# Optimization experiments

Measured on AMD Instinct MI355X. Metric: run time of the kernel, lower is better.

## Reference

```python
import jax, jax.numpy as jnp
import numpy as np

B, S, D, H = 2, 2048, 1024, 16
HD = D // H  # head_dim = 64


def setup_inputs() -> dict:
    key = jax.random.key(0)
    k1, k2, k3 = jax.random.split(key, 3)
    x = jax.random.normal(k1, (B, S, D), dtype=jnp.float32)
    W_qkv = jax.random.normal(k2, (D, 3 * D), dtype=jnp.float32) * (D ** -0.5)
    b_qkv = jnp.zeros((3 * D,), dtype=jnp.float32)
    W_proj = jax.random.normal(k3, (D, D), dtype=jnp.float32) * (D ** -0.5)
    b_proj = jnp.zeros((D,), dtype=jnp.float32)
    return {"x": x, "W_qkv": W_qkv, "b_qkv": b_qkv, "W_proj": W_proj, "b_proj": b_proj}


def reference(x, W_qkv, b_qkv, W_proj, b_proj):
    b, s, d = x.shape
    scale = HD ** -0.5
    qkv = x @ W_qkv + b_qkv                       # [B,S,3D]
    q, k, v = jnp.split(qkv, 3, axis=-1)
    # [B,S,D] -> [B,H,S,HD]
    def to_heads(t):
        return t.reshape(b, s, H, HD).transpose(0, 2, 1, 3)
    q, k, v = map(to_heads, (q, k, v))
    scores = jnp.einsum('bhqd,bhkd->bhqk', q, k) * scale  # [B,H,S,S]
    causal = jnp.triu(jnp.ones((s, s), dtype=bool), k=1)
    scores = jnp.where(causal[None, None], -jnp.inf, scores)
    attn = jax.nn.softmax(scores, axis=-1)
    out = jnp.einsum('bhqk,bhkd->bhqd', attn, v)  # [B,H,S,HD]
    out = out.transpose(0, 2, 1, 3).reshape(b, s, d)
    return out @ W_proj + b_proj
```

## Files before the change

### kernel.cpp

```cpp
#include <hip/hip_runtime.h>

using frag_t = __attribute__((ext_vector_type(8))) short;
using f32x4  = __attribute__((ext_vector_type(4))) float;

#define L2E 1.4426950408889634f

#if __has_builtin(__builtin_amdgcn_exp2f)
#define EXP2(x) __builtin_amdgcn_exp2f(x)
#else
#define EXP2(x) exp2f(x)
#endif

constexpr int B_  = 2, S_ = 2048, D_ = 1024, H_ = 16, HD_ = 64;
constexpr int M_  = B_ * S_;
constexpr float QSCALE = 0.125f * L2E;

__device__ __forceinline__ ushort f2bf(float f) {
  union { float f; unsigned u; } v; v.f = f;
  unsigned u = v.u;
  unsigned r = (u + 0x7FFFu + ((u >> 16) & 1u)) >> 16;
  return (ushort)r;
}
__device__ __forceinline__ unsigned pk_bf2(float a, float b) {
  unsigned ua = __float_as_uint(a) + 0x8000u;
  unsigned ub = __float_as_uint(b) + 0x8000u;
  return (ua >> 16) | (ub & 0xFFFF0000u);
}

__device__ __forceinline__ void gld_lds16(const ushort* g, ushort* l) {
  __builtin_amdgcn_global_load_lds((const __attribute__((address_space(1))) void*)g,
                                   (__attribute__((address_space(3))) void*)l, 16, 0, 0);
}

__global__ __launch_bounds__(256) void k_prep(
    const float* __restrict__ x, const float* __restrict__ Wqkv,
    const float* __restrict__ Wproj,
    ushort* __restrict__ Xbf, ushort* __restrict__ Wqt, ushort* __restrict__ Wpt) {
  int blk = blockIdx.x, tid = threadIdx.x;
  if (blk < 1024) {
    size_t base = (size_t)blk * 4096 + tid * 4;
    #pragma unroll
    for (int i = 0; i < 4; ++i) {
      float4 f = *(const float4*)(x + base + i * 1024);
      ushort4 o;
      o.x = f2bf(f.x); o.y = f2bf(f.y); o.z = f2bf(f.z); o.w = f2bf(f.w);
      *(ushort4*)(Xbf + base + i * 1024) = o;
    }
  } else {
    __shared__ float tile[64][65];
    const float* in; ushort* out; int N, K, bx, by;
    if (blk < 1024 + 768) { int b2 = blk - 1024; in = Wqkv;  out = Wqt; N = 3072; K = 1024; bx = b2 % 48; by = b2 / 48; }
    else                  { int b2 = blk - 1792; in = Wproj; out = Wpt; N = 1024; K = 1024; bx = b2 % 16; by = b2 / 16; }
    int n0 = bx * 64, k0 = by * 64;
    int tx = tid & 63, ty = tid >> 6;
    #pragma unroll
    for (int i = 0; i < 16; ++i)
      tile[ty + i * 4][tx] = in[(size_t)(k0 + ty + i * 4) * N + n0 + tx];
    __syncthreads();
    #pragma unroll
    for (int i = 0; i < 16; ++i)
      out[(size_t)(n0 + ty + i * 4) * K + k0 + tx] = f2bf(tile[tx][ty + i * 4]);
  }
}

template <int EPI>
__global__ __launch_bounds__(256) void k_gemm(
    const ushort* __restrict__ A, const ushort* __restrict__ Bt,
    const float* __restrict__ bias,
    ushort* __restrict__ Qo, ushort* __restrict__ Ko, ushort* __restrict__ Vo,
    float* __restrict__ Co, int N, int K) {
  constexpr int BM = (EPI == 0) ? 128 : 64;
  constexpr int BN = 64, BK = 64;
  constexpr int MI = (EPI == 0) ? 4 : 2, NI = 2;
  __shared__ ushort smem[(BM + BN) * BK];
  ushort* As = smem;
  ushort* Bs = smem + BM * BK;
  int tid  = threadIdx.x;
  int lane = tid & 63, wave = tid >> 6;
  int quad = lane >> 4, li = lane & 15;
  int mbase = (wave >> 1) * (MI * 16);
  int nbase = (wave & 1) * 32;
  int m0 = blockIdx.y * BM, n0 = blockIdx.x * BN;
  int srow = lane >> 3;
  int scol = ((lane & 7) ^ srow) * 8;
  f32x4 acc[MI][NI] = {};
  for (int k0 = 0; k0 < K; k0 += BK) {
    if (EPI == 0) {
      #pragma unroll
      for (int i = 0; i < 4; ++i) {
        int rbase = i * 32 + wave * 8;
        gld_lds16(&A[(size_t)(m0 + rbase + srow) * K + k0 + scol], &As[rbase * BK]);
      }
    } else {
      #pragma unroll
      for (int i = 0; i < 2; ++i) {
        int rbase = wave * 16 + i * 8;
        gld_lds16(&A[(size_t)(m0 + rbase + srow) * K + k0 + scol], &As[rbase * BK]);
      }
    }
    #pragma unroll
    for (int i = 0; i < 2; ++i) {
      int rbase = wave * 16 + i * 8;
      gld_lds16(&Bt[(size_t)(n0 + rbase + srow) * K + k0 + scol], &Bs[rbase * BK]);
    }
    __syncthreads();
    #pragma unroll
    for (int ks = 0; ks < 2; ++ks) {
      frag_t af[MI], bf[NI];
      #pragma unroll
      for (int mi = 0; mi < MI; ++mi)
        af[mi] = *(const frag_t*)&As[(mbase + mi * 16 + li) * BK + (((ks * 4 + quad) ^ (li & 7)) * 8)];
      #pragma unroll
      for (int ni = 0; ni < NI; ++ni)
        bf[ni] = *(const frag_t*)&Bs[(nbase + ni * 16 + li) * BK + (((ks * 4 + quad) ^ (li & 7)) * 8)];
      #pragma unroll
      for (int mi = 0; mi < MI; ++mi)
        #pragma unroll
        for (int ni = 0; ni < NI; ++ni)
          acc[mi][ni] = __builtin_amdgcn_mfma_f32_16x16x32_bf16(af[mi], bf[ni], acc[mi][ni], 0, 0, 0);
    }
    __syncthreads();
  }
  if (EPI == 1) {
    #pragma unroll
    for (int mi = 0; mi < MI; ++mi)
      #pragma unroll
      for (int ni = 0; ni < NI; ++ni) {
        int gcol = n0 + nbase + ni * 16 + li;
        float bv = bias[gcol];
        #pragma unroll
        for (int r = 0; r < 4; ++r) {
          int grow = m0 + mbase + mi * 16 + quad * 4 + r;
          Co[(size_t)grow * N + gcol] = acc[mi][ni][r] + bv;
        }
      }
  } else {
    int which = (n0 + nbase) >> 10;
    if (which < 2) {
      #pragma unroll
      for (int mi = 0; mi < MI; ++mi)
        #pragma unroll
        for (int ni = 0; ni < NI; ++ni) {
          int gcol = n0 + nbase + ni * 16 + li;
          float bv = bias[gcol];
          #pragma unroll
          for (int r = 0; r < 4; ++r) {
            int grow = m0 + mbase + mi * 16 + quad * 4 + r;
            float v = acc[mi][ni][r] + bv;
            int d = gcol & 1023, h = d >> 6, hd = d & 63;
            int b = grow >> 11, s = grow & 2047;
            size_t bh = (size_t)b * H_ + h;
            if (which == 0) Qo[(bh * S_ + s) * HD_ + hd] = f2bf(v * QSCALE);
            else            Ko[(bh * S_ + s) * HD_ + hd] = f2bf(v);
          }
        }
    } else {
      ushort* vlds = smem + wave * (32 * 72);
      #pragma unroll
      for (int ni = 0; ni < NI; ++ni) {
        float bv = bias[n0 + nbase + ni * 16 + li];
        #pragma unroll
        for (int mi = 0; mi < MI; ++mi)
          #pragma unroll
          for (int r = 0; r < 4; ++r)
            vlds[(ni * 16 + li) * 72 + 16 * quad + 4 * r + mi] = f2bf(acc[mi][ni][r] + bv);
      }
      int hgrp = (((n0 & 1023) + nbase) >> 6);
      int hd0  = (n0 + nbase) & 63;
      int b = m0 >> 11;
      int s0 = (m0 & 2047) + mbase;
      size_t vbase = (size_t)(b * H_ + hgrp) * HD_ * S_;
      #pragma unroll
      for (int i = 0; i < 4; ++i) {
        int row = i * 8 + (lane >> 3);
        int col = (lane & 7) * 8;
        *(uint4*)&Vo[vbase + (size_t)(hd0 + row) * S_ + s0 + col] = *(const uint4*)&vlds[row * 72 + col];
      }
    }
  }
}

__global__ __launch_bounds__(256) void k_attn(
    const ushort* __restrict__ Q, const ushort* __restrict__ K,
    const ushort* __restrict__ Vt, ushort* __restrict__ O) {
  __shared__ ushort Kbuf[2][64 * 64];
  __shared__ ushort Vbuf[2][64 * 64];
  __shared__ ushort Plds[4 * 16 * 64];
  int lane = threadIdx.x & 63, wave = threadIdx.x >> 6;
  int quad = lane >> 4, li = lane & 15;
  int bh = blockIdx.x;
  int qb = 31 - (int)blockIdx.y;
  int b = bh >> 4, h = bh & 15;
  int q0 = qb * 64 + wave * 16;
  const ushort* Qb = Q  + (size_t)bh * S_ * HD_;
  const ushort* Kb = K  + (size_t)bh * S_ * HD_;
  const ushort* Vb = Vt + (size_t)bh * HD_ * S_;
  ushort* Pw = &Plds[wave * 1024];

  frag_t qf[2];
  #pragma unroll
  for (int ks = 0; ks < 2; ++ks)
    qf[ks] = *(const frag_t*)&Qb[(size_t)(q0 + li) * HD_ + ks * 32 + quad * 8];

  frag_t ones;
  #pragma unroll
  for (int i = 0; i < 8; ++i) ones[i] = (short)0x3F80;

  f32x4 o[4] = {};
  f32x4 lacc = {};

  auto stage = [&](int kb, int bi) {
    #pragma unroll
    for (int i = 0; i < 2; ++i) {
      int rt  = wave * 16 + i * 8 + (lane >> 3);
      int c16 = (lane & 7) ^ (lane >> 3);
      gld_lds16(&Kb[(size_t)(kb * 64 + rt) * HD_ + c16 * 8], &Kbuf[bi][(wave * 16 + i * 8) * 64]);
      gld_lds16(&Vb[(size_t)rt * S_ + kb * 64 + c16 * 8],    &Vbuf[bi][(wave * 16 + i * 8) * 64]);
    }
  };

  auto comp = [&](int kb, bool diag, int bi) {
    f32x4 sc[4];
    #pragma unroll
    for (int t = 0; t < 4; ++t) {
      f32x4 a = {};
      #pragma unroll
      for (int ks = 0; ks < 2; ++ks) {
        frag_t kf = *(const frag_t*)&Kbuf[bi][(t * 16 + li) * 64 + (((quad + ks * 4) ^ (li & 7)) * 8)];
        a = __builtin_amdgcn_mfma_f32_16x16x32_bf16(qf[ks], kf, a, 0, 0, 0);
      }
      sc[t] = a;
    }
    if (diag) {
      #pragma unroll
      for (int t = 0; t < 4; ++t) {
        int key = kb * 64 + t * 16 + li;
        #pragma unroll
        for (int r = 0; r < 4; ++r)
          if (key > q0 + quad * 4 + r) sc[t][r] = -1e30f;
      }
    }
    #pragma unroll
    for (int t = 0; t < 4; ++t)
      #pragma unroll
      for (int r = 0; r < 4; ++r)
        sc[t][r] = EXP2(sc[t][r]);
    #pragma unroll
    for (int r = 0; r < 4; ++r) {
      int row = quad * 4 + r;
      uint2 w;
      w.x = pk_bf2(sc[0][r], sc[1][r]);
      w.y = pk_bf2(sc[2][r], sc[3][r]);
      *(uint2*)&Pw[row * 64 + ((li ^ (row & 6)) * 4)] = w;
    }
    frag_t pf[2];
    #pragma unroll
    for (int ks = 0; ks < 2; ++ks) {
      int g0 = (ks * 4 + quad) * 2;
      pf[ks] = *(const frag_t*)&Pw[li * 64 + ((g0 ^ (li & 6)) * 4)];
    }
    lacc = __builtin_amdgcn_mfma_f32_16x16x32_bf16(pf[0], ones, lacc, 0, 0, 0);
    lacc = __builtin_amdgcn_mfma_f32_16x16x32_bf16(pf[1], ones, lacc, 0, 0, 0);
    #pragma unroll
    for (int t = 0; t < 4; ++t)
      #pragma unroll
      for (int ks = 0; ks < 2; ++ks) {
        frag_t vf = *(const frag_t*)&Vbuf[bi][(t * 16 + li) * 64 + (((quad + ks * 4) ^ (li & 7)) * 8)];
        o[t] = __builtin_amdgcn_mfma_f32_16x16x32_bf16(pf[ks], vf, o[t], 0, 0, 0);
      }
  };

  stage(0, 0);
  __syncthreads();
  for (int kb = 0; kb <= qb; ++kb) {
    if (kb < qb) stage(kb + 1, (kb + 1) & 1);
    comp(kb, kb == qb, kb & 1);
    __syncthreads();
  }

  #pragma unroll
  for (int r = 0; r < 4; ++r) {
    float inv = 1.f / lacc[r];
    int srow = q0 + quad * 4 + r;
    #pragma unroll
    for (int ht = 0; ht < 4; ++ht)
      O[((size_t)b * S_ + srow) * D_ + h * 64 + ht * 16 + li] = f2bf(o[ht][r] * inv);
  }
}

extern "C" void kernel_launch(void* const* d_in, const int* in_sizes, int n_in,
                              void* d_out, int out_size, void* d_ws, size_t ws_size,
                              hipStream_t stream) {
  (void)in_sizes; (void)n_in; (void)out_size; (void)ws_size;
  const float* x     = (const float*)d_in[0];
  const float* Wqkv  = (const float*)d_in[1];
  const float* bqkv  = (const float*)d_in[2];
  const float* Wproj = (const float*)d_in[3];
  const float* bproj = (const float*)d_in[4];
  float* out = (float*)d_out;

  char* ws = (char*)d_ws;
  ushort* Xbf = (ushort*)(ws);
  ushort* Wqt = (ushort*)(ws + (8u  << 20));
  ushort* Wpt = (ushort*)(ws + (14u << 20));
  ushort* Qbf = (ushort*)(ws + (16u << 20));
  ushort* Kbf = (ushort*)(ws + (24u << 20));
  ushort* Vtb = (ushort*)(ws + (32u << 20));
  ushort* Obf = Xbf;

  k_prep<<<dim3(2048), dim3(256), 0, stream>>>(x, Wqkv, Wproj, Xbf, Wqt, Wpt);
  k_gemm<0><<<dim3(48, 32), dim3(256), 0, stream>>>(Xbf, Wqt, bqkv, Qbf, Kbf, Vtb,
                                                    (float*)nullptr, 3 * D_, D_);
  k_attn<<<dim3(B_ * H_, 32), dim3(256), 0, stream>>>(Qbf, Kbf, Vtb, Obf);
  k_gemm<1><<<dim3(16, 64), dim3(256), 0, stream>>>(Obf, Wpt, bproj,
                                                    (ushort*)nullptr, (ushort*)nullptr, (ushort*)nullptr,
                                                    out, D_, D_);
}
```

Before: 172.0 us.

## Replace QKV GEMM with 256x256-tile 8-wave pipelined kernel using direct LDS loads

Adds a new QKV projection kernel that computes 256x256 output tiles with 8 waves and 512 threads. It double-buffers K-slices in LDS via direct global-to-LDS loads with an XOR swizzle, and interleaves staging with MFMA phases under explicit waitcnt, barriers and setprio. Workgroups are remapped so neighbours share A/B tiles in L2. The goal is more data reuse and better compute/load overlap than the 128x64 tile kernel, at the cost of 128KB of LDS, heavy register use, and only 192 workgroups.

Measured after the change: 170.1 us. Within noise of the previous version (-1.1%).

```diff
diff --git a/kernel.cpp b/kernel.cpp
--- a/kernel.cpp
+++ b/kernel.cpp
@@ -60,6 +60,131 @@
     #pragma unroll
     for (int i = 0; i < 16; ++i)
       out[(size_t)(n0 + ty + i * 4) * K + k0 + tx] = f2bf(tile[tx][ty + i * 4]);
+  }
+}
+
+__global__ __launch_bounds__(512, 2) void k_gemm8(
+    const ushort* __restrict__ A, const ushort* __restrict__ Bt,
+    const float* __restrict__ bias,
+    ushort* __restrict__ Qo, ushort* __restrict__ Ko, ushort* __restrict__ Vo) {
+  __shared__ ushort smem[65536];
+  int tid = threadIdx.x;
+  int lane = tid & 63, wave = tid >> 6;
+  int quad = lane >> 4, li = lane & 15;
+  int wm = wave >> 2, wn = wave & 3;
+  int wg = blockIdx.x;
+  int swz = (wg & 7) * 24 + (wg >> 3);
+  int by = swz / 12, bx = swz % 12;
+  int m0 = by * 256, n0 = bx * 256;
+  const ushort* Asrc = A  + (size_t)m0 * 1024;
+  const ushort* Bsrc = Bt + (size_t)n0 * 1024;
+  int srow   = lane >> 2;
+  int schunk = (lane & 3) ^ ((lane >> 4) & 3);
+  int pos    = (quad ^ ((li >> 2) & 3)) * 8;
+
+#define STG(BI, ISB, KS, KT) do { \
+    const ushort* _s = (ISB) ? Bsrc : Asrc; \
+    ushort* _d = &smem[((BI)*4 + (ISB)*2 + (KS)) * 8192]; \
+    _Pragma("unroll") \
+    for (int j = 0; j < 2; ++j) \
+      gld_lds16(&_s[(size_t)(j*128 + wave*16 + srow) * 1024 + (KT)*64 + (KS)*32 + schunk*8], \
+                &_d[(j*128 + wave*16) * 32]); \
+  } while (0)
+
+  f32x4 acc[8][4] = {};
+  frag_t af[8], bf[2];
+
+#define PH(BI, KS, NH, STGS, W4) do { \
+    if ((NH) == 0) { \
+      _Pragma("unroll") \
+      for (int mi = 0; mi < 8; ++mi) \
+        af[mi] = *(const frag_t*)&smem[((BI)*4 + (KS)) * 8192 + (wm*128 + mi*16 + li) * 32 + pos]; \
+    } \
+    _Pragma("unroll") \
+    for (int nj = 0; nj < 2; ++nj) \
+      bf[nj] = *(const frag_t*)&smem[((BI)*4 + 2 + (KS)) * 8192 + (wn*64 + ((NH)*2 + nj)*16 + li) * 32 + pos]; \
+    STGS; \
+    if (W4) asm volatile("s_waitcnt vmcnt(4)" ::: "memory"); \
+    asm volatile("s_barrier" ::: "memory"); \
+    __builtin_amdgcn_s_setprio(1); \
+    _Pragma("unroll") \
+    for (int mi = 0; mi < 8; ++mi) { \
+      acc[mi][(NH)*2+0] = __builtin_amdgcn_mfma_f32_16x16x32_bf16(af[mi], bf[0], acc[mi][(NH)*2+0], 0, 0, 0); \
+      acc[mi][(NH)*2+1] = __builtin_amdgcn_mfma_f32_16x16x32_bf16(af[mi], bf[1], acc[mi][(NH)*2+1], 0, 0, 0); \
+    } \
+    __builtin_amdgcn_s_setprio(0); \
+    asm volatile("s_barrier" ::: "memory"); \
+  } while (0)
+
+  STG(0,0,0,0); STG(0,1,0,0); STG(0,0,1,0); STG(0,1,1,0);
+  STG(1,0,0,1); STG(1,1,0,1);
+  asm volatile("s_waitcnt vmcnt(4)" ::: "memory");
+  asm volatile("s_barrier" ::: "memory");
+
+  for (int it = 0; it < 8; ++it) {
+    int t1 = 2*it + 1;
+    int t2 = (2*it + 2 < 16) ? 2*it + 2 : 15;
+    int t3 = (2*it + 3 < 16) ? 2*it + 3 : 15;
+    PH(0,0,0, STG(1,0,1,t1), 0);
+    PH(0,0,1, STG(1,1,1,t1), 0);
+    PH(0,1,0, STG(0,0,0,t2), 0);
+    PH(0,1,1, STG(0,1,0,t2), 1);
+    PH(1,0,0, STG(0,0,1,t2), 0);
+    PH(1,0,1, STG(0,1,1,t2), 0);
+    PH(1,1,0, STG(1,0,0,t3), 0);
+    PH(1,1,1, STG(1,1,0,t3), 1);
+  }
+#undef PH
+#undef STG
+
+  asm volatile("s_waitcnt vmcnt(0)" ::: "memory");
+  __syncthreads();
+
+  int which = (n0 + wn * 64) >> 10;
+  if (which < 2) {
+    #pragma unroll
+    for (int ni = 0; ni < 4; ++ni) {
+      int gcol = n0 + wn * 64 + ni * 16 + li;
+      float bv = bias[gcol];
+      int d = gcol & 1023, h = d >> 6, hd = d & 63;
+      #pragma unroll
+      for (int mi = 0; mi < 8; ++mi)
+        #pragma unroll
+        for (int r = 0; r < 4; ++r) {
+          int grow = m0 + wm * 128 + mi * 16 + quad * 4 + r;
+          int b = grow >> 11, s = grow & 2047;
+          size_t off = (((size_t)b * H_ + h) * S_ + s) * HD_ + hd;
+          float v = acc[mi][ni][r] + bv;
+          if (which == 0) Qo[off] = f2bf(v * QSCALE);
+          else            Ko[off] = f2bf(v);
+        }
+    }
+  } else {
+    ushort* vl = &smem[wave * 8192];
+    #pragma unroll
+    for (int ni = 0; ni < 4; ++ni) {
+      int row = ni * 16 + li;
+      float bv = bias[n0 + wn * 64 + row];
+      int rx = (row & 7) << 3;
+      #pragma unroll
+      for (int mi = 0; mi < 8; ++mi)
+        #pragma unroll
+        for (int r = 0; r < 4; ++r) {
+          int col = (mi >> 2) * 64 + quad * 16 + r * 4 + (mi & 3);
+          vl[row * 128 + (col ^ rx)] = f2bf(acc[mi][ni][r] + bv);
+        }
+    }
+    int h  = ((n0 & 1023) + wn * 64) >> 6;
+    int b  = m0 >> 11;
+    int s0 = (m0 & 2047) + wm * 128;
+    size_t vbase = ((size_t)b * H_ + h) * HD_ * S_;
+    #pragma unroll
+    for (int i = 0; i < 16; ++i) {
+      int row = i * 4 + quad;
+      int col = li * 8;
+      *(uint4*)&Vo[vbase + (size_t)row * S_ + s0 + col] =
+          *(const uint4*)&vl[row * 128 + (col ^ ((row & 7) << 3))];
+    }
   }
 }
 
@@ -134,49 +259,6 @@
           Co[(size_t)grow * N + gcol] = acc[mi][ni][r] + bv;
         }
       }
-  } else {
-    int which = (n0 + nbase) >> 10;
-    if (which < 2) {
-      #pragma unroll
-      for (int mi = 0; mi < MI; ++mi)
-        #pragma unroll
-        for (int ni = 0; ni < NI; ++ni) {
-          int gcol = n0 + nbase + ni * 16 + li;
-          float bv = bias[gcol];
-          #pragma unroll
-          for (int r = 0; r < 4; ++r) {
-            int grow = m0 + mbase + mi * 16 + quad * 4 + r;
-            float v = acc[mi][ni][r] + bv;
-            int d = gcol & 1023, h = d >> 6, hd = d & 63;
-            int b = grow >> 11, s = grow & 2047;
-            size_t bh = (size_t)b * H_ + h;
-            if (which == 0) Qo[(bh * S_ + s) * HD_ + hd] = f2bf(v * QSCALE);
-            else            Ko[(bh * S_ + s) * HD_ + hd] = f2bf(v);
-          }
-        }
-    } else {
-      ushort* vlds = smem + wave * (32 * 72);
-      #pragma unroll
-      for (int ni = 0; ni < NI; ++ni) {
-        float bv = bias[n0 + nbase + ni * 16 + li];
-        #pragma unroll
-        for (int mi = 0; mi < MI; ++mi)
-          #pragma unroll
-          for (int r = 0; r < 4; ++r)
-            vlds[(ni * 16 + li) * 72 + 16 * quad + 4 * r + mi] = f2bf(acc[mi][ni][r] + bv);
-      }
-      int hgrp = (((n0 & 1023) + nbase) >> 6);
-      int hd0  = (n0 + nbase) & 63;
-      int b = m0 >> 11;
-      int s0 = (m0 & 2047) + mbase;
-      size_t vbase = (size_t)(b * H_ + hgrp) * HD_ * S_;
-      #pragma unroll
-      for (int i = 0; i < 4; ++i) {
-        int row = i * 8 + (lane >> 3);
-        int col = (lane & 7) * 8;
-        *(uint4*)&Vo[vbase + (size_t)(hd0 + row) * S_ + s0 + col] = *(const uint4*)&vlds[row * 72 + col];
-      }
-    }
   }
 }
 
@@ -309,8 +391,7 @@
   ushort* Obf = Xbf;
 
   k_prep<<<dim3(2048), dim3(256), 0, stream>>>(x, Wqkv, Wproj, Xbf, Wqt, Wpt);
-  k_gemm<0><<<dim3(48, 32), dim3(256), 0, stream>>>(Xbf, Wqt, bqkv, Qbf, Kbf, Vtb,
-                                                    (float*)nullptr, 3 * D_, D_);
+  k_gemm8<<<dim3(192), dim3(512), 0, stream>>>(Xbf, Wqt, bqkv, Qbf, Kbf, Vtb);
   k_attn<<<dim3(B_ * H_, 32), dim3(256), 0, stream>>>(Qbf, Kbf, Vtb, Obf);
   k_gemm<1><<<dim3(16, 64), dim3(256), 0, stream>>>(Obf, Wpt, bproj,
                                                     (ushort*)nullptr, (ushort*)nullptr, (ushort*)nullptr,
```
